# Optimization experiments

Measured on AMD Instinct MI355X. Metric: run time of the kernel, lower is better.

Reference implementation:

```python
import jax, jax.numpy as jnp
import numpy as np

DIM = 1024
DIM_HEAD = 64
HEADS = 16
BATCH = 2
SEQ = 2048
SCALE = DIM_HEAD ** -0.5


def setup_inputs() -> dict:
    key = jax.random.key(0)
    ks = jax.random.split(key, 5)
    tokens = jax.random.normal(ks[0], (BATCH, SEQ, DIM), dtype=jnp.float32)
    wq = jax.random.normal(ks[1], (HEADS, DIM, DIM_HEAD), dtype=jnp.float32)
    wk = jax.random.normal(ks[2], (HEADS, DIM, DIM_HEAD), dtype=jnp.float32)
    wv = jax.random.normal(ks[3], (HEADS, DIM, DIM_HEAD), dtype=jnp.float32)
    wo = jax.random.normal(ks[4], (HEADS, DIM_HEAD, DIM), dtype=jnp.float32)
    return {"tokens": tokens, "wq": wq, "wk": wk, "wv": wv, "wo": wo}


def reference(tokens, wq, wk, wv, wo):
    # q, k, v: [b, h, n, dh]
    q = jnp.einsum('bnd,hde->bhne', tokens, wq) * SCALE
    k = jnp.einsum('bnd,hde->bhne', tokens, wk)
    v = jnp.einsum('bnd,hde->bhne', tokens, wv)
    sim = jnp.einsum('bhie,bhje->bhij', q, k)          # [b, h, n, n]
    attn = jax.nn.softmax(sim, axis=-1)
    aggregated = jnp.einsum('bhij,bhje->bhie', attn, v)  # [b, h, n, dh]
    retrieved = jnp.einsum('bhne,hed->bnd', aggregated, wo)  # sum over heads
    return retrieved
```

## Files before the change

### kernel.cpp

```cpp
#include <hip/hip_runtime.h>
#include <hip/hip_fp16.h>
#include <stdint.h>

#define BB 2
#define HH 16
#define SS 2048
#define DD 1024
#define DHH 64
#define QSCALE 0.18033688011112042f

typedef _Float16 half8 __attribute__((ext_vector_type(8)));
typedef _Float16 half4 __attribute__((ext_vector_type(4)));
typedef __fp16 fp16x2 __attribute__((ext_vector_type(2)));
typedef float floatx4 __attribute__((ext_vector_type(4)));

__device__ __forceinline__ floatx4 mfma16(half8 a, half8 b, floatx4 c) {
  return __builtin_amdgcn_mfma_f32_16x16x32_f16(a, b, c, 0, 0, 0);
}

__device__ __forceinline__ void dma16(const _Float16* g, _Float16* l) {
  __builtin_amdgcn_global_load_lds(
      (const __attribute__((address_space(1))) uint32_t*)g,
      (__attribute__((address_space(3))) uint32_t*)l,
      16, 0, 0);
}


__global__ __launch_bounds__(256) void convert_kernel(
    const float* __restrict__ wq, const float* __restrict__ wk,
    const float* __restrict__ wv, const float* __restrict__ wo,
    _Float16* __restrict__ Wh, _Float16* __restrict__ Wl,
    _Float16* __restrict__ Wot)
{
  __shared__ float St[64][68];
  const int kt = blockIdx.x;
  const int hy = blockIdx.y;
  const int z  = blockIdx.z;
  const int t  = (int)threadIdx.x;
  const int k0 = kt * 64;

  const float* src = (z == 0) ? (wq + hy * (DD * DHH))
                   : (z == 1) ? (wk + hy * (DD * DHH))
                   : (z == 2) ? (wv + hy * (DD * DHH))
                   : wo;

  const int rr = t >> 4, cc = (t & 15) * 4;
  if (z < 3) {
    #pragma unroll
    for (int i = 0; i < 4; ++i)
      *(floatx4*)&St[rr + 16 * i][cc] =
          *(const floatx4*)(src + (k0 + rr + 16 * i) * DHH + cc);
  } else {
    const int d0 = hy * 64;
    #pragma unroll
    for (int i = 0; i < 4; ++i)
      *(floatx4*)&St[rr + 16 * i][cc] =
          *(const floatx4*)(src + (k0 + rr + 16 * i) * 1024 + d0 + cc);
  }
  __syncthreads();

  const int e = t >> 2, kc = (t & 3) * 16;
  if (z < 3) {
    const int n = z * 1024 + hy * 64 + e;
    half8 hi0, hi1, lo0, lo1;
    #pragma unroll
    for (int u = 0; u < 16; ++u) {
      float x = St[kc + u][e];
      _Float16 hh = (_Float16)x;
      _Float16 ll = (_Float16)(x - (float)hh);
      if (u < 8) { hi0[u] = hh; lo0[u] = ll; }
      else       { hi1[u - 8] = hh; lo1[u - 8] = ll; }
    }
    *(half8*)(Wh + n * 1024 + k0 + kc)     = hi0;
    *(half8*)(Wh + n * 1024 + k0 + kc + 8) = hi1;
    *(half8*)(Wl + n * 1024 + k0 + kc)     = lo0;
    *(half8*)(Wl + n * 1024 + k0 + kc + 8) = lo1;
  } else {
    const int d0 = hy * 64;
    half8 hi0, hi1;
    #pragma unroll
    for (int u = 0; u < 16; ++u) {
      _Float16 hh = (_Float16)St[kc + u][e];
      if (u < 8) hi0[u] = hh; else hi1[u - 8] = hh;
    }
    *(half8*)(Wot + (d0 + e) * 1024 + k0 + kc)     = hi0;
    *(half8*)(Wot + (d0 + e) * 1024 + k0 + kc + 8) = hi1;
  }
}

__global__ __launch_bounds__(256) void tokens_split_kernel(
    const float* __restrict__ tokens,
    _Float16* __restrict__ th, _Float16* __restrict__ tl)
{
  const int i = ((int)blockIdx.x * 256 + (int)threadIdx.x) * 8;
  floatx4 x0 = *(const floatx4*)(tokens + i);
  floatx4 x1 = *(const floatx4*)(tokens + i + 4);
  half8 h, l;
  #pragma unroll
  for (int j = 0; j < 8; ++j) {
    float x = (j < 4) ? x0[j] : x1[j - 4];
    _Float16 hh = (_Float16)x;
    h[j] = hh;
    l[j] = (_Float16)(x - (float)hh);
  }
  *(half8*)(th + i) = h;
  *(half8*)(tl + i) = l;
}

__global__ __launch_bounds__(256) void qkv_gemm_kernel(
    const _Float16* __restrict__ th, const _Float16* __restrict__ tl,
    const _Float16* __restrict__ Wh, const _Float16* __restrict__ Wl,
    _Float16* __restrict__ qh, _Float16* __restrict__ ql,
    _Float16* __restrict__ kh, _Float16* __restrict__ kl,
    _Float16* __restrict__ vt)
{
  __shared__ alignas(16) _Float16 sAh[128 * 32];
  __shared__ alignas(16) _Float16 sAl[128 * 32];
  __shared__ alignas(16) _Float16 sBh[128 * 32];
  __shared__ alignas(16) _Float16 sBl[128 * 32];

  const int n0 = blockIdx.x * 128;
  const int m0 = blockIdx.y * 128;
  const int zb = n0 >> 10;
  const bool is_v = (zb == 2);
  const int t = (int)threadIdx.x;
  const int lane = t & 63, wid = t >> 6;
  const int l16 = lane & 15, q4 = lane >> 4;
  const int mw = (wid & 1) * 64, nw = (wid >> 1) * 64;

  const int g  = (lane & 7) ^ ((lane >> 3) & 7);
  const int grow  = (lane >> 3) * 2 + (g >> 2);
  const int gcol8 = (g & 3) * 8;

  const int laneoff = (l16 >> 1) * 128 + (((((l16 & 1) << 2) | q4) ^ (l16 >> 1)) * 16);

  const _Float16* src;
  _Float16* dst;
  if (wid == 0)      { src = th + m0 * 1024; dst = sAh; }
  else if (wid == 1) { src = Wh + n0 * 1024; dst = sBh; }
  else if (wid == 2) { src = Wl + n0 * 1024; dst = sBl; }
  else               { src = tl + m0 * 1024; dst = sAl; }
  const bool stage_active = !(is_v && wid == 3);
  const _Float16* gsrc = src + grow * 1024 + gcol8;

  const floatx4 z4 = {0.0f, 0.0f, 0.0f, 0.0f};
  floatx4 acc[4][4];
  #pragma unroll
  for (int mi = 0; mi < 4; ++mi)
    #pragma unroll
    for (int ni = 0; ni < 4; ++ni) acc[mi][ni] = z4;

  for (int kt = 0; kt < 32; ++kt) {
    __syncthreads();
    if (stage_active) {
      const _Float16* gp = gsrc + kt * 32;
      #pragma unroll
      for (int j = 0; j < 8; ++j)
        dma16(gp + j * 16 * 1024, dst + j * 16 * 32);
    }
    __syncthreads();

    half8 a_h[4];
    #pragma unroll
    for (int mi = 0; mi < 4; ++mi)
      a_h[mi] = *(const half8*)((const char*)sAh + (mw + mi * 16) * 64 + laneoff);
    if (!is_v) {
      half8 a_l[4];
      #pragma unroll
      for (int mi = 0; mi < 4; ++mi)
        a_l[mi] = *(const half8*)((const char*)sAl + (mw + mi * 16) * 64 + laneoff);
      #pragma unroll
      for (int ni = 0; ni < 4; ++ni) {
        const half8 b_h = *(const half8*)((const char*)sBh + (nw + ni * 16) * 64 + laneoff);
        const half8 b_l = *(const half8*)((const char*)sBl + (nw + ni * 16) * 64 + laneoff);
        #pragma unroll
        for (int mi = 0; mi < 4; ++mi) {
          acc[mi][ni] = mfma16(a_h[mi], b_h, acc[mi][ni]);
          acc[mi][ni] = mfma16(a_h[mi], b_l, acc[mi][ni]);
          acc[mi][ni] = mfma16(a_l[mi], b_h, acc[mi][ni]);
        }
      }
    } else {
      #pragma unroll
      for (int ni = 0; ni < 4; ++ni) {
        const half8 b_h = *(const half8*)((const char*)sBh + (nw + ni * 16) * 64 + laneoff);
        const half8 b_l = *(const half8*)((const char*)sBl + (nw + ni * 16) * 64 + laneoff);
        #pragma unroll
        for (int mi = 0; mi < 4; ++mi) {
          acc[mi][ni] = mfma16(a_h[mi], b_h, acc[mi][ni]);
          acc[mi][ni] = mfma16(a_h[mi], b_l, acc[mi][ni]);
        }
      }
    }
  }

  #pragma unroll
  for (int ni = 0; ni < 4; ++ni) {
    const int ncol = n0 + nw + ni * 16;
    const int h = (ncol >> 6) & 15;
    const int e = (ncol & 63) + l16;
    #pragma unroll
    for (int mi = 0; mi < 4; ++mi) {
      #pragma unroll
      for (int r = 0; r < 4; ++r) {
        const int grow2 = m0 + mw + mi * 16 + q4 * 4 + r;
        const int b = grow2 >> 11, s = grow2 & 2047;
        const float v = acc[mi][ni][r];
        const int qkidx = ((b * HH + h) * SS + s) * DHH + e;
        if (zb == 0) {
          const float vs = v * QSCALE;
          const _Float16 hh = (_Float16)vs;
          qh[qkidx] = hh;
          ql[qkidx] = (_Float16)(vs - (float)hh);
        } else if (zb == 1) {
          const _Float16 hh = (_Float16)v;
          kh[qkidx] = hh;
          kl[qkidx] = (_Float16)(v - (float)hh);
        } else {
          vt[((b * HH + h) * DHH + e) * SS + s] = (_Float16)v;
        }
      }
    }
  }
}

__global__ __launch_bounds__(512) void attn_kernel(
    const _Float16* __restrict__ qh, const _Float16* __restrict__ ql,
    const _Float16* __restrict__ kh, const _Float16* __restrict__ kl,
    const _Float16* __restrict__ vt, _Float16* __restrict__ agg)
{
  __shared__ _Float16 Kh[64][72], Kl[64][72], Vs[64][72];
  __shared__ _Float16 Ps[128][72];

  const int qt = blockIdx.x;
  const int h  = blockIdx.y;
  const int b  = blockIdx.z;
  const int bh = b * HH + h;
  const int t = (int)threadIdx.x;
  const int lane = t & 63, wid = t >> 6;
  const int l16 = lane & 15, q4 = lane >> 4;

  const int sr = t >> 3, sc = (t & 7) * 8;

  half8 qfh[2], qfl[2];
  {
    const int s = qt * 128 + wid * 16 + l16;
    const int base = (bh * SS + s) * DHH + q4 * 8;
    qfh[0] = *(const half8*)(qh + base);
    qfh[1] = *(const half8*)(qh + base + 32);
    qfl[0] = *(const half8*)(ql + base);
    qfl[1] = *(const half8*)(ql + base + 32);
  }

  const floatx4 z4 = {0.0f, 0.0f, 0.0f, 0.0f};
  floatx4 o[4];
  #pragma unroll
  for (int i = 0; i < 4; ++i) o[i] = z4;
  float m_r = -1e30f, l_r = 0.0f;

  half8 pK, pL, pV;
  {
    const int gk = (bh * SS + sr) * DHH + sc;
    pK = *(const half8*)(kh + gk);
    pL = *(const half8*)(kl + gk);
    pV = *(const half8*)(vt + (bh * DHH + sr) * SS + sc);
  }

  for (int kt = 0; kt < 32; ++kt) {
    __syncthreads();
    *(half8*)&Kh[sr][sc] = pK;
    *(half8*)&Kl[sr][sc] = pL;
    *(half8*)&Vs[sr][sc] = pV;
    __syncthreads();

    if (kt < 31) {
      const int k1 = (kt + 1) * 64;
      const int gk = (bh * SS + k1 + sr) * DHH + sc;
      pK = *(const half8*)(kh + gk);
      pL = *(const half8*)(kl + gk);
      pV = *(const half8*)(vt + (bh * DHH + sr) * SS + k1 + sc);
    }

    floatx4 sv[4];
    #pragma unroll
    for (int sub = 0; sub < 4; ++sub) {
      const half8 ah0 = *(const half8*)&Kh[sub * 16 + l16][q4 * 8];
      const half8 ah1 = *(const half8*)&Kh[sub * 16 + l16][q4 * 8 + 32];
      const half8 al0 = *(const half8*)&Kl[sub * 16 + l16][q4 * 8];
      const half8 al1 = *(const half8*)&Kl[sub * 16 + l16][q4 * 8 + 32];
      floatx4 s4 = z4;
      s4 = mfma16(ah0, qfh[0], s4);
      s4 = mfma16(ah1, qfh[1], s4);
      s4 = mfma16(al0, qfh[0], s4);
      s4 = mfma16(al1, qfh[1], s4);
      s4 = mfma16(ah0, qfl[0], s4);
      s4 = mfma16(ah1, qfl[1], s4);
      sv[sub] = s4;
    }

    float mx = fmaxf(fmaxf(sv[0][0], sv[0][1]), fmaxf(sv[0][2], sv[0][3]));
    #pragma unroll
    for (int sub = 1; sub < 4; ++sub)
      mx = fmaxf(mx, fmaxf(fmaxf(sv[sub][0], sv[sub][1]),
                           fmaxf(sv[sub][2], sv[sub][3])));
    mx = fmaxf(mx, __shfl_xor(mx, 16));
    mx = fmaxf(mx, __shfl_xor(mx, 32));
    const float mnew = fmaxf(m_r, mx);

    float psum = 0.0f;
    #pragma unroll
    for (int sub = 0; sub < 4; ++sub) {
      #pragma unroll
      for (int r = 0; r < 4; ++r) {
        float p = exp2f(sv[sub][r] - mnew);
        sv[sub][r] = p;
        psum += p;
      }
    }

    #pragma unroll
    for (int sub = 0; sub < 4; ++sub) {
      fp16x2 p01 = __builtin_amdgcn_cvt_pkrtz(sv[sub][0], sv[sub][1]);
      fp16x2 p23 = __builtin_amdgcn_cvt_pkrtz(sv[sub][2], sv[sub][3]);
      half4 pv;
      pv[0] = (_Float16)p01[0]; pv[1] = (_Float16)p01[1];
      pv[2] = (_Float16)p23[0]; pv[3] = (_Float16)p23[1];
      *(half4*)&Ps[wid * 16 + l16][sub * 16 + q4 * 4] = pv;
    }

    psum += __shfl_xor(psum, 16);
    psum += __shfl_xor(psum, 32);

    if (__any(mnew > m_r)) {
      const float alpha = exp2f(m_r - mnew);
      l_r = l_r * alpha + psum;
      m_r = mnew;
      #pragma unroll
      for (int sub = 0; sub < 4; ++sub)
        #pragma unroll
        for (int r = 0; r < 4; ++r) o[sub][r] *= alpha;
    } else {
      l_r += psum;
    }

    asm volatile("s_waitcnt lgkmcnt(0)" ::: "memory");

    const half8 pb0 = *(const half8*)&Ps[wid * 16 + l16][q4 * 8];
    const half8 pb1 = *(const half8*)&Ps[wid * 16 + l16][q4 * 8 + 32];
    #pragma unroll
    for (int sub = 0; sub < 4; ++sub) {
      const half8 va0 = *(const half8*)&Vs[sub * 16 + l16][q4 * 8];
      const half8 va1 = *(const half8*)&Vs[sub * 16 + l16][q4 * 8 + 32];
      o[sub] = mfma16(va0, pb0, o[sub]);
      o[sub] = mfma16(va1, pb1, o[sub]);
    }
  }

  const float inv = 1.0f / l_r;
  const int s = qt * 128 + wid * 16 + l16;
  #pragma unroll
  for (int sub = 0; sub < 4; ++sub) {
    half4 ov;
    #pragma unroll
    for (int r = 0; r < 4; ++r) ov[r] = (_Float16)(o[sub][r] * inv);
    *(half4*)(agg + (b * SS + s) * (HH * DHH) + h * DHH + sub * 16 + q4 * 4) = ov;
  }
}

__global__ __launch_bounds__(256) void out_gemm_kernel(
    const _Float16* __restrict__ agg, const _Float16* __restrict__ Wot,
    float* __restrict__ out)
{
  __shared__ alignas(16) _Float16 sA[128 * 32];
  __shared__ alignas(16) _Float16 sB[128 * 32];
  const int n0 = blockIdx.x * 128;
  const int m0 = blockIdx.y * 128;
  const int t = (int)threadIdx.x;
  const int lane = t & 63, wid = t >> 6;
  const int l16 = lane & 15, q4 = lane >> 4;
  const int mw = (wid & 1) * 64, nw = (wid >> 1) * 64;

  const int g  = (lane & 7) ^ ((lane >> 3) & 7);
  const int grow  = (lane >> 3) * 2 + (g >> 2);
  const int gcol8 = (g & 3) * 8;
  const int laneoff = (l16 >> 1) * 128 + (((((l16 & 1) << 2) | q4) ^ (l16 >> 1)) * 16);

  const _Float16* src = (wid < 2) ? (agg + m0 * 1024) : (Wot + n0 * 1024);
  _Float16* dst = (wid < 2) ? sA : sB;
  const int half64 = (wid & 1) * 64;
  const _Float16* gsrc = src + (half64 + grow) * 1024 + gcol8;
  _Float16* ldst = dst + half64 * 32;

  const floatx4 z4 = {0.0f, 0.0f, 0.0f, 0.0f};
  floatx4 acc[4][4];
  #pragma unroll
  for (int mi = 0; mi < 4; ++mi)
    #pragma unroll
    for (int ni = 0; ni < 4; ++ni) acc[mi][ni] = z4;

  for (int kt = 0; kt < 32; ++kt) {
    __syncthreads();
    {
      const _Float16* gp = gsrc + kt * 32;
      #pragma unroll
      for (int j = 0; j < 4; ++j)
        dma16(gp + j * 16 * 1024, ldst + j * 16 * 32);
    }
    __syncthreads();

    half8 a_f[4];
    #pragma unroll
    for (int mi = 0; mi < 4; ++mi)
      a_f[mi] = *(const half8*)((const char*)sA + (mw + mi * 16) * 64 + laneoff);
    #pragma unroll
    for (int ni = 0; ni < 4; ++ni) {
      const half8 b_f = *(const half8*)((const char*)sB + (nw + ni * 16) * 64 + laneoff);
      #pragma unroll
      for (int mi = 0; mi < 4; ++mi)
        acc[mi][ni] = mfma16(a_f[mi], b_f, acc[mi][ni]);
    }
  }

  #pragma unroll
  for (int ni = 0; ni < 4; ++ni)
    #pragma unroll
    for (int mi = 0; mi < 4; ++mi)
      #pragma unroll
      for (int r = 0; r < 4; ++r)
        out[(m0 + mw + mi * 16 + q4 * 4 + r) * 1024 + n0 + nw + ni * 16 + l16] =
            acc[mi][ni][r];
}

extern "C" void kernel_launch(void* const* d_in, const int* in_sizes, int n_in,
                              void* d_out, int out_size, void* d_ws, size_t ws_size,
                              hipStream_t stream)
{
  const float* tokens = (const float*)d_in[0];
  const float* wq = (const float*)d_in[1];
  const float* wk = (const float*)d_in[2];
  const float* wv = (const float*)d_in[3];
  const float* wo = (const float*)d_in[4];
  float* out = (float*)d_out;

  char* ws = (char*)d_ws;
  _Float16* qh  = (_Float16*)(ws);
  _Float16* ql  = (_Float16*)(ws + 8388608);
  _Float16* kh  = (_Float16*)(ws + 16777216);
  _Float16* kl  = (_Float16*)(ws + 25165824);
  _Float16* vt  = (_Float16*)(ws + 33554432);
  _Float16* Wh  = (_Float16*)(ws + 41943040);
  _Float16* Wl  = (_Float16*)(ws + 48234496);
  _Float16* Wot = (_Float16*)(ws + 54525952);
  _Float16* th  = (_Float16*)(ws + 56623104);
  _Float16* tl  = (_Float16*)(ws + 65011712);
  _Float16* agg = (_Float16*)(ws + 56623104);

  convert_kernel<<<dim3(16, 16, 4), 256, 0, stream>>>(wq, wk, wv, wo, Wh, Wl, Wot);
  tokens_split_kernel<<<2048, 256, 0, stream>>>(tokens, th, tl);
  qkv_gemm_kernel<<<dim3(24, 32), 256, 0, stream>>>(th, tl, Wh, Wl, qh, ql, kh, kl, vt);
  attn_kernel<<<dim3(16, 16, 2), 512, 0, stream>>>(qh, ql, kh, kl, vt, agg);
  out_gemm_kernel<<<dim3(8, 32), 256, 0, stream>>>(agg, Wot, out);
}
```

Measured before the change: 303.8 us.

## Double-buffer LDS tiles in QKV and output projection GEMMs

```diff
diff --git a/kernel.cpp b/kernel.cpp
--- a/kernel.cpp
+++ b/kernel.cpp
@@ -114,10 +114,7 @@
     _Float16* __restrict__ kh, _Float16* __restrict__ kl,
     _Float16* __restrict__ vt)
 {
-  __shared__ alignas(16) _Float16 sAh[128 * 32];
-  __shared__ alignas(16) _Float16 sAl[128 * 32];
-  __shared__ alignas(16) _Float16 sBh[128 * 32];
-  __shared__ alignas(16) _Float16 sBl[128 * 32];
+  __shared__ alignas(16) _Float16 sbuf[2][4][128 * 32];
 
   const int n0 = blockIdx.x * 128;
   const int m0 = blockIdx.y * 128;
@@ -131,15 +128,14 @@
   const int g  = (lane & 7) ^ ((lane >> 3) & 7);
   const int grow  = (lane >> 3) * 2 + (g >> 2);
   const int gcol8 = (g & 3) * 8;
-
   const int laneoff = (l16 >> 1) * 128 + (((((l16 & 1) << 2) | q4) ^ (l16 >> 1)) * 16);
 
   const _Float16* src;
-  _Float16* dst;
-  if (wid == 0)      { src = th + m0 * 1024; dst = sAh; }
-  else if (wid == 1) { src = Wh + n0 * 1024; dst = sBh; }
-  else if (wid == 2) { src = Wl + n0 * 1024; dst = sBl; }
-  else               { src = tl + m0 * 1024; dst = sAl; }
+  int arr;
+  if (wid == 0)      { src = th + m0 * 1024; arr = 0; }
+  else if (wid == 1) { src = Wh + n0 * 1024; arr = 1; }
+  else if (wid == 2) { src = Wl + n0 * 1024; arr = 2; }
+  else               { src = tl + m0 * 1024; arr = 3; }
   const bool stage_active = !(is_v && wid == 3);
   const _Float16* gsrc = src + grow * 1024 + gcol8;
 
@@ -150,29 +146,34 @@
     #pragma unroll
     for (int ni = 0; ni < 4; ++ni) acc[mi][ni] = z4;
 
-  for (int kt = 0; kt < 32; ++kt) {
-    __syncthreads();
+  auto stage = [&](int buf, int kt2) {
     if (stage_active) {
-      const _Float16* gp = gsrc + kt * 32;
+      const _Float16* gp = gsrc + kt2 * 32;
+      _Float16* dst = &sbuf[buf][arr][0];
       #pragma unroll
       for (int j = 0; j < 8; ++j)
         dma16(gp + j * 16 * 1024, dst + j * 16 * 32);
     }
-    __syncthreads();
-
+  };
+
+  auto compute = [&](int buf) {
+    const char* sAh = (const char*)&sbuf[buf][0][0];
+    const char* sBh = (const char*)&sbuf[buf][1][0];
+    const char* sBl = (const char*)&sbuf[buf][2][0];
+    const char* sAl = (const char*)&sbuf[buf][3][0];
     half8 a_h[4];
     #pragma unroll
     for (int mi = 0; mi < 4; ++mi)
-      a_h[mi] = *(const half8*)((const char*)sAh + (mw + mi * 16) * 64 + laneoff);
+      a_h[mi] = *(const half8*)(sAh + (mw + mi * 16) * 64 + laneoff);
     if (!is_v) {
       half8 a_l[4];
       #pragma unroll
       for (int mi = 0; mi < 4; ++mi)
-        a_l[mi] = *(const half8*)((const char*)sAl + (mw + mi * 16) * 64 + laneoff);
+        a_l[mi] = *(const half8*)(sAl + (mw + mi * 16) * 64 + laneoff);
       #pragma unroll
       for (int ni = 0; ni < 4; ++ni) {
-        const half8 b_h = *(const half8*)((const char*)sBh + (nw + ni * 16) * 64 + laneoff);
-        const half8 b_l = *(const half8*)((const char*)sBl + (nw + ni * 16) * 64 + laneoff);
+        const half8 b_h = *(const half8*)(sBh + (nw + ni * 16) * 64 + laneoff);
+        const half8 b_l = *(const half8*)(sBl + (nw + ni * 16) * 64 + laneoff);
         #pragma unroll
         for (int mi = 0; mi < 4; ++mi) {
           acc[mi][ni] = mfma16(a_h[mi], b_h, acc[mi][ni]);
@@ -183,8 +184,8 @@
     } else {
       #pragma unroll
       for (int ni = 0; ni < 4; ++ni) {
-        const half8 b_h = *(const half8*)((const char*)sBh + (nw + ni * 16) * 64 + laneoff);
-        const half8 b_l = *(const half8*)((const char*)sBl + (nw + ni * 16) * 64 + laneoff);
+        const half8 b_h = *(const half8*)(sBh + (nw + ni * 16) * 64 + laneoff);
+        const half8 b_l = *(const half8*)(sBl + (nw + ni * 16) * 64 + laneoff);
         #pragma unroll
         for (int mi = 0; mi < 4; ++mi) {
           acc[mi][ni] = mfma16(a_h[mi], b_h, acc[mi][ni]);
@@ -192,6 +193,19 @@
         }
       }
     }
+  };
+
+  stage(0, 0);
+  __syncthreads();
+
+  #pragma unroll 1
+  for (int kt = 0; kt < 32; kt += 2) {
+    if (kt + 1 < 32) stage(1, kt + 1);
+    compute(0);
+    __syncthreads();
+    if (kt + 2 < 32) stage(0, kt + 2);
+    compute(1);
+    __syncthreads();
   }
 
   #pragma unroll
@@ -371,8 +385,7 @@
     const _Float16* __restrict__ agg, const _Float16* __restrict__ Wot,
     float* __restrict__ out)
 {
-  __shared__ alignas(16) _Float16 sA[128 * 32];
-  __shared__ alignas(16) _Float16 sB[128 * 32];
+  __shared__ alignas(16) _Float16 sbuf[2][2][128 * 32];
   const int n0 = blockIdx.x * 128;
   const int m0 = blockIdx.y * 128;
   const int t = (int)threadIdx.x;
@@ -385,11 +398,10 @@
   const int gcol8 = (g & 3) * 8;
   const int laneoff = (l16 >> 1) * 128 + (((((l16 & 1) << 2) | q4) ^ (l16 >> 1)) * 16);
 
-  const _Float16* src = (wid < 2) ? (agg + m0 * 1024) : (Wot + n0 * 1024);
-  _Float16* dst = (wid < 2) ? sA : sB;
+  const int arr = wid >> 1;
   const int half64 = (wid & 1) * 64;
+  const _Float16* src = (arr == 0) ? (agg + m0 * 1024) : (Wot + n0 * 1024);
   const _Float16* gsrc = src + (half64 + grow) * 1024 + gcol8;
-  _Float16* ldst = dst + half64 * 32;
 
   const floatx4 z4 = {0.0f, 0.0f, 0.0f, 0.0f};
   floatx4 acc[4][4];
@@ -398,27 +410,41 @@
     #pragma unroll
     for (int ni = 0; ni < 4; ++ni) acc[mi][ni] = z4;
 
-  for (int kt = 0; kt < 32; ++kt) {
-    __syncthreads();
-    {
-      const _Float16* gp = gsrc + kt * 32;
-      #pragma unroll
-      for (int j = 0; j < 4; ++j)
-        dma16(gp + j * 16 * 1024, ldst + j * 16 * 32);
-    }
-    __syncthreads();
-
+  auto stage = [&](int buf, int kt2) {
+    const _Float16* gp = gsrc + kt2 * 32;
+    _Float16* dst = &sbuf[buf][arr][half64 * 32];
+    #pragma unroll
+    for (int j = 0; j < 4; ++j)
+      dma16(gp + j * 16 * 1024, dst + j * 16 * 32);
+  };
+
+  auto compute = [&](int buf) {
+    const char* sA = (const char*)&sbuf[buf][0][0];
+    const char* sB = (const char*)&sbuf[buf][1][0];
     half8 a_f[4];
     #pragma unroll
     for (int mi = 0; mi < 4; ++mi)
-      a_f[mi] = *(const half8*)((const char*)sA + (mw + mi * 16) * 64 + laneoff);
+      a_f[mi] = *(const half8*)(sA + (mw + mi * 16) * 64 + laneoff);
     #pragma unroll
     for (int ni = 0; ni < 4; ++ni) {
-      const half8 b_f = *(const half8*)((const char*)sB + (nw + ni * 16) * 64 + laneoff);
+      const half8 b_f = *(const half8*)(sB + (nw + ni * 16) * 64 + laneoff);
       #pragma unroll
       for (int mi = 0; mi < 4; ++mi)
         acc[mi][ni] = mfma16(a_f[mi], b_f, acc[mi][ni]);
     }
+  };
+
+  stage(0, 0);
+  __syncthreads();
+
+  #pragma unroll 1
+  for (int kt = 0; kt < 32; kt += 2) {
+    if (kt + 1 < 32) stage(1, kt + 1);
+    compute(0);
+    __syncthreads();
+    if (kt + 2 < 32) stage(0, kt + 2);
+    compute(1);
+    __syncthreads();
   }
 
   #pragma unroll
```

Result: faster. 272.5 us (-10.3%).
